# Kernel optimization log

Hardware: AMD Instinct MI355X
Metric: run time of the kernel (lower is better)

The kernel has to match this reference:

```python
import jax, jax.numpy as jnp
import numpy as np

N, E = 50000, 800000
NODE_DIM, EDGE_DIM, HIDDEN = 128, 32, 128


def setup_inputs() -> dict:
    key = jax.random.key(0)
    ks = jax.random.split(key, 12)
    def lin(k, fan_in, shape):
        bound = 1.0 / np.sqrt(fan_in)
        return jax.random.uniform(k, shape, jnp.float32, -bound, bound)
    return {
        "x": jax.random.normal(ks[0], (N, NODE_DIM), jnp.float32),
        "edge_index": jax.random.randint(ks[1], (2, E), 0, N),
        "edge_attr": jax.random.normal(ks[2], (E, EDGE_DIM), jnp.float32),
        # msg MLP: Linear(node+edge -> hidden), Linear(hidden -> hidden)
        "W1": lin(ks[3], NODE_DIM + EDGE_DIM, (HIDDEN, NODE_DIM + EDGE_DIM)),
        "b1": lin(ks[4], NODE_DIM + EDGE_DIM, (HIDDEN,)),
        "W2": lin(ks[5], HIDDEN, (HIDDEN, HIDDEN)),
        "b2": lin(ks[6], HIDDEN, (HIDDEN,)),
        # GRUCell(input=HIDDEN, hidden=NODE_DIM); gate order r,z,n (torch)
        "W_ih": lin(ks[7], NODE_DIM, (3 * NODE_DIM, HIDDEN)),
        "b_ih": lin(ks[8], NODE_DIM, (3 * NODE_DIM,)),
        "W_hh": lin(ks[9], NODE_DIM, (3 * NODE_DIM, NODE_DIM)),
        "b_hh": lin(ks[10], NODE_DIM, (3 * NODE_DIM,)),
    }


def reference(x, edge_index, edge_attr, W1, b1, W2, b2, W_ih, b_ih, W_hh, b_hh):
    src, dst = edge_index[0], edge_index[1]
    # gather + edge MLP: [E, node+edge] -> [E, hidden]
    m_in = jnp.concatenate([x[src], edge_attr], axis=-1)
    h1 = jax.nn.silu(m_in @ W1.T + b1)
    m = jax.nn.silu(h1 @ W2.T + b2)
    # scatter-add messages per destination node
    agg = jax.ops.segment_sum(m, dst, num_segments=x.shape[0])  # [N, hidden]
    # GRUCell: gates in torch order (r, z, n)
    gi = agg @ W_ih.T + b_ih  # [N, 3*node_dim]
    gh = x @ W_hh.T + b_hh
    i_r, i_z, i_n = jnp.split(gi, 3, axis=-1)
    h_r, h_z, h_n = jnp.split(gh, 3, axis=-1)
    r = jax.nn.sigmoid(i_r + h_r)
    z = jax.nn.sigmoid(i_z + h_z)
    n = jnp.tanh(i_n + r * h_n)
    return (1.0 - z) * n + z * x
```

## Files before the change

kernel.cpp:

```cpp
#include <hip/hip_runtime.h>
#include <hip/hip_bf16.h>
#include <cstdint>

typedef __bf16 bf16x8 __attribute__((ext_vector_type(8)));
typedef __bf16 bf16x4 __attribute__((ext_vector_type(4)));
typedef float  f32x4  __attribute__((ext_vector_type(4)));

#define ND 128
#define HID 128

__device__ __forceinline__ f32x4 mfma_bf16(bf16x8 a, bf16x8 b, f32x4 c) {
  return __builtin_amdgcn_mfma_f32_16x16x32_bf16(a, b, c, 0, 0, 0);
}
__device__ __forceinline__ float fast_sigmoid(float x) {
  return __fdividef(1.f, 1.f + __expf(-x));
}
__device__ __forceinline__ float fast_silu(float x) {
  return __fdividef(x, 1.f + __expf(-x));
}
__device__ __forceinline__ float fast_tanh(float x) {
  float cx = fminf(fmaxf(x, -15.f), 15.f);
  float e = __expf(2.f * cx);
  return __fdividef(e - 1.f, e + 1.f);
}

__global__ void cvt_f32_bf16(const float* __restrict__ src, __bf16* __restrict__ dst, int n8) {
  int i = blockIdx.x * blockDim.x + threadIdx.x;
  if (i >= n8) return;
  const float4* s = reinterpret_cast<const float4*>(src) + (size_t)i * 2;
  float4 a = s[0], b = s[1];
  bf16x8 v;
  v[0] = (__bf16)a.x; v[1] = (__bf16)a.y; v[2] = (__bf16)a.z; v[3] = (__bf16)a.w;
  v[4] = (__bf16)b.x; v[5] = (__bf16)b.y; v[6] = (__bf16)b.z; v[7] = (__bf16)b.w;
  reinterpret_cast<bf16x8*>(dst)[i] = v;
}

__global__ void k_hist(const int* __restrict__ dst, int* __restrict__ counts, int E) {
  int e = blockIdx.x * 256 + threadIdx.x;
  if (e < E) atomicAdd(&counts[dst[e]], 1);
}

__global__ void k_blocksum(const int* __restrict__ counts, int* __restrict__ bsum) {
  __shared__ int sd[256];
  int t = threadIdx.x;
  sd[t] = counts[blockIdx.x * 256 + t];
  __syncthreads();
  for (int d = 128; d > 0; d >>= 1) { if (t < d) sd[t] += sd[t + d]; __syncthreads(); }
  if (!t) bsum[blockIdx.x] = sd[0];
}

__global__ void k_scan_bsum(int* __restrict__ bsum, int nb) {
  __shared__ int sd[256];
  int t = threadIdx.x;
  int v = (t < nb) ? bsum[t] : 0;
  sd[t] = v;
  __syncthreads();
  for (int d = 1; d < 256; d <<= 1) {
    int u = (t >= d) ? sd[t - d] : 0;
    __syncthreads();
    sd[t] += u;
    __syncthreads();
  }
  if (t < nb) bsum[t] = sd[t] - v;
}

__global__ void k_scan_write(const int* __restrict__ counts, const int* __restrict__ bsum,
                             int* __restrict__ offsets, int* __restrict__ cursor) {
  __shared__ int sd[256];
  int t = threadIdx.x, b = blockIdx.x;
  int i = b * 256 + t;
  int c = counts[i];
  sd[t] = c;
  __syncthreads();
  for (int d = 1; d < 256; d <<= 1) {
    int u = (t >= d) ? sd[t - d] : 0;
    __syncthreads();
    sd[t] += u;
    __syncthreads();
  }
  int excl = bsum[b] + sd[t] - c;
  offsets[i] = excl;
  cursor[i]  = excl;
  if (b == (int)gridDim.x - 1 && t == 255) offsets[i + 1] = excl + c;
}

__global__ void k_spos(const int* __restrict__ dst, int* __restrict__ cursor,
                       int* __restrict__ spos, int E) {
  int e = blockIdx.x * 256 + threadIdx.x;
  if (e < E) spos[e] = atomicAdd(&cursor[dst[e]], 1);
}

#define TILE_E 64
#define A_PAD 168
#define H_PAD 136

template <int SORT>
__global__ __launch_bounds__(512) void edge_mlp(
    const __bf16* __restrict__ xb,
    const int*    __restrict__ ei,
    const float*  __restrict__ ea,
    const __bf16* __restrict__ W1b,
    const float*  __restrict__ b1,
    const __bf16* __restrict__ W2b,
    const float*  __restrict__ b2,
    float*  __restrict__ agg,
    __bf16* __restrict__ mbuf,
    const int* __restrict__ spos,
    int E, int ntiles)
{
  __shared__ __bf16 Als[TILE_E][A_PAD];
  __shared__ __bf16 H1ls[TILE_E][H_PAD];
  __shared__ int sposls[TILE_E];

  const int tid = threadIdx.x;
  const int w  = tid >> 6;
  const int l  = tid & 63;
  const int l4 = l >> 4;
  const int lm = l & 15;
  const int jw = w * 16 + lm;

  bf16x8 bw1[5];
#pragma unroll
  for (int kt = 0; kt < 5; ++kt)
    bw1[kt] = *reinterpret_cast<const bf16x8*>(W1b + (size_t)jw * 160 + kt * 32 + l4 * 8);
  bf16x8 bw2[4];
#pragma unroll
  for (int kt = 0; kt < 4; ++kt)
    bw2[kt] = *reinterpret_cast<const bf16x8*>(W2b + (size_t)jw * 128 + kt * 32 + l4 * 8);
  const float b1v = b1[jw];
  const float b2v = b2[jw];
  const int* srcp = ei;
  const int* dstp = ei + E;

  __bf16* Mls = &Als[0][0];

  for (int tile = blockIdx.x; tile < ntiles; tile += gridDim.x) {
    const int e0 = tile * TILE_E;

#pragma unroll
    for (int it = 0; it < 2; ++it) {
      int idx = it * 512 + tid;
      int e = idx >> 4, q = idx & 15;
      int s = srcp[e0 + e];
      bf16x8 v = *reinterpret_cast<const bf16x8*>(xb + (size_t)s * ND + q * 8);
      *reinterpret_cast<bf16x8*>(&Als[e][q * 8]) = v;
    }
    {
      int e = tid >> 3, q = tid & 7;
      float4 v = reinterpret_cast<const float4*>(ea)[(size_t)(e0 + e) * 8 + q];
      bf16x4 h;
      h[0] = (__bf16)v.x; h[1] = (__bf16)v.y; h[2] = (__bf16)v.z; h[3] = (__bf16)v.w;
      *reinterpret_cast<bf16x4*>(&Als[e][ND + q * 4]) = h;
    }
    if (SORT && tid < TILE_E) sposls[tid] = spos[e0 + tid];
    __syncthreads();

#pragma unroll
    for (int rt = 0; rt < 4; ++rt) {
      const int er = rt * 16;
      f32x4 acc = {0.f, 0.f, 0.f, 0.f};
#pragma unroll
      for (int kt = 0; kt < 5; ++kt) {
        bf16x8 a = *reinterpret_cast<const bf16x8*>(&Als[er + lm][kt * 32 + l4 * 8]);
        acc = mfma_bf16(a, bw1[kt], acc);
      }
#pragma unroll
      for (int rr = 0; rr < 4; ++rr) {
        float hv = fast_silu(acc[rr] + b1v);
        H1ls[er + l4 * 4 + rr][jw] = (__bf16)hv;
      }
    }
    __syncthreads();

#pragma unroll
    for (int rt = 0; rt < 4; ++rt) {
      const int er = rt * 16;
      f32x4 acc = {0.f, 0.f, 0.f, 0.f};
#pragma unroll
      for (int kt = 0; kt < 4; ++kt) {
        bf16x8 a = *reinterpret_cast<const bf16x8*>(&H1ls[er + lm][kt * 32 + l4 * 8]);
        acc = mfma_bf16(a, bw2[kt], acc);
      }
      if (SORT) {
#pragma unroll
        for (int rr = 0; rr < 4; ++rr) {
          float mv = fast_silu(acc[rr] + b2v);
          Mls[(er + l4 * 4 + rr) * H_PAD + jw] = (__bf16)mv;
        }
      } else {
#pragma unroll
        for (int rr = 0; rr < 4; ++rr) {
          float mv = fast_silu(acc[rr] + b2v);
          int d = dstp[e0 + er + l4 * 4 + rr];
          atomicAdd(agg + (size_t)d * HID + jw, mv);
        }
      }
    }
    __syncthreads();

    if (SORT) {
#pragma unroll
      for (int it = 0; it < 2; ++it) {
        int idx = it * 512 + tid;
        int row = idx >> 4, q = idx & 15;
        bf16x8 v = *reinterpret_cast<const bf16x8*>(&Mls[row * H_PAD + q * 8]);
        int sp = sposls[row];
        *reinterpret_cast<bf16x8*>(mbuf + (size_t)sp * HID + q * 8) = v;
      }
      __syncthreads();
    }
  }
}

__global__ __launch_bounds__(256) void k_aggregate(
    const __bf16* __restrict__ mbuf, const int* __restrict__ offsets,
    __bf16* __restrict__ aggb, int N)
{
  int node = blockIdx.x * 4 + (threadIdx.x >> 6);
  int l = threadIdx.x & 63;
  if (node >= N) return;
  int lo = offsets[node], hi = offsets[node + 1];
  float s0 = 0.f, s1 = 0.f;
  const uint32_t* p = reinterpret_cast<const uint32_t*>(mbuf) + (size_t)lo * 64 + l;
  int r = lo;
  for (; r + 1 < hi; r += 2) {
    uint32_t v0 = p[0];
    uint32_t v1 = p[64];
    p += 128;
    s0 += __uint_as_float(v0 << 16);
    s1 += __uint_as_float(v0 & 0xffff0000u);
    s0 += __uint_as_float(v1 << 16);
    s1 += __uint_as_float(v1 & 0xffff0000u);
  }
  if (r < hi) {
    uint32_t v0 = p[0];
    s0 += __uint_as_float(v0 << 16);
    s1 += __uint_as_float(v0 & 0xffff0000u);
  }
  uint32_t o = (uint32_t)__builtin_bit_cast(unsigned short, (__bf16)s0) |
               ((uint32_t)__builtin_bit_cast(unsigned short, (__bf16)s1) << 16);
  reinterpret_cast<uint32_t*>(aggb)[(size_t)node * 64 + l] = o;
}

__global__ __launch_bounds__(512) void gru2(
    const __bf16* __restrict__ aggb,
    const __bf16* __restrict__ xb,
    const float*  __restrict__ x,
    const __bf16* __restrict__ Wih, const float* __restrict__ bih,
    const __bf16* __restrict__ Whh, const float* __restrict__ bhh,
    float* __restrict__ out, int N)
{
  const int tid = threadIdx.x;
  const int w = tid >> 6, l = tid & 63;
  const int l4 = l >> 4, lm = l & 15;
  const int n0 = blockIdx.x * 64;
  const int jr = w * 16 + lm, jz = jr + 128, jn = jr + 256;

  bf16x8 WiR[4], WhR[4], WiZ[4], WhZ[4], WiN[4], WhN[4];
#pragma unroll
  for (int kt = 0; kt < 4; ++kt) {
    int ko = kt * 32 + l4 * 8;
    WiR[kt] = *reinterpret_cast<const bf16x8*>(Wih + (size_t)jr * ND + ko);
    WhR[kt] = *reinterpret_cast<const bf16x8*>(Whh + (size_t)jr * ND + ko);
    WiZ[kt] = *reinterpret_cast<const bf16x8*>(Wih + (size_t)jz * ND + ko);
    WhZ[kt] = *reinterpret_cast<const bf16x8*>(Whh + (size_t)jz * ND + ko);
    WiN[kt] = *reinterpret_cast<const bf16x8*>(Wih + (size_t)jn * ND + ko);
    WhN[kt] = *reinterpret_cast<const bf16x8*>(Whh + (size_t)jn * ND + ko);
  }
  const float bir = bih[jr] + bhh[jr];
  const float biz = bih[jz] + bhh[jz];
  const float bin = bih[jn], bhn = bhh[jn];

#pragma unroll
  for (int rt = 0; rt < 4; ++rt) {
    int na = n0 + rt * 16 + lm;
    bf16x8 aA[4], aX[4];
#pragma unroll
    for (int kt = 0; kt < 4; ++kt) {
      int ko = kt * 32 + l4 * 8;
      bf16x8 z8 = {};
      aA[kt] = (na < N) ? *reinterpret_cast<const bf16x8*>(aggb + (size_t)na * ND + ko) : z8;
      aX[kt] = (na < N) ? *reinterpret_cast<const bf16x8*>(xb + (size_t)na * ND + ko) : z8;
    }
    f32x4 aR = {0.f,0.f,0.f,0.f}, aZ = {0.f,0.f,0.f,0.f};
    f32x4 ai = {0.f,0.f,0.f,0.f}, ah = {0.f,0.f,0.f,0.f};
#pragma unroll
    for (int kt = 0; kt < 4; ++kt) {
      aR = mfma_bf16(aA[kt], WiR[kt], aR);
      aR = mfma_bf16(aX[kt], WhR[kt], aR);
      aZ = mfma_bf16(aA[kt], WiZ[kt], aZ);
      aZ = mfma_bf16(aX[kt], WhZ[kt], aZ);
      ai = mfma_bf16(aA[kt], WiN[kt], ai);
      ah = mfma_bf16(aX[kt], WhN[kt], ah);
    }
#pragma unroll
    for (int rr = 0; rr < 4; ++rr) {
      int node = n0 + rt * 16 + l4 * 4 + rr;
      if (node < N) {
        float r = fast_sigmoid(aR[rr] + bir);
        float z = fast_sigmoid(aZ[rr] + biz);
        float n = fast_tanh(ai[rr] + bin + r * (ah[rr] + bhn));
        float xv = x[(size_t)node * ND + jr];
        out[(size_t)node * ND + jr] = (1.f - z) * n + z * xv;
      }
    }
  }
}

extern "C" void kernel_launch(void* const* d_in, const int* in_sizes, int n_in,
                              void* d_out, int out_size, void* d_ws, size_t ws_size,
                              hipStream_t stream) {
  const float* x   = (const float*)d_in[0];
  const int*   ei  = (const int*)d_in[1];
  const float* ea  = (const float*)d_in[2];
  const float* W1  = (const float*)d_in[3];
  const float* b1  = (const float*)d_in[4];
  const float* W2  = (const float*)d_in[5];
  const float* b2  = (const float*)d_in[6];
  const float* Wih = (const float*)d_in[7];
  const float* bih = (const float*)d_in[8];
  const float* Whh = (const float*)d_in[9];
  const float* bhh = (const float*)d_in[10];
  float* out = (float*)d_out;
  const int N = in_sizes[0] / ND;
  const int E = in_sizes[1] / 2;

  const int nb = (N + 255) / 256;
  const int nC = nb * 256;

  char* ws = (char*)d_ws;
  size_t off = 0;
  auto alloc = [&](size_t bytes) -> void* {
    void* p = ws + off;
    off += (bytes + 255) & ~(size_t)255;
    return p;
  };
  __bf16* xb   = (__bf16*)alloc((size_t)N * ND * 2);
  __bf16* aggb = (__bf16*)alloc((size_t)N * ND * 2);
  __bf16* W1b  = (__bf16*)alloc(128 * 160 * 2);
  __bf16* W2b  = (__bf16*)alloc(128 * 128 * 2);
  __bf16* Wihb = (__bf16*)alloc(384 * 128 * 2);
  __bf16* Whhb = (__bf16*)alloc(384 * 128 * 2);
  size_t common_off = off;

  int*    counts  = (int*)alloc((size_t)nC * 4);
  int*    offsets = (int*)alloc((size_t)(nC + 16) * 4);
  int*    cursor  = (int*)alloc((size_t)nC * 4);
  int*    bsum    = (int*)alloc(256 * 4);
  int*    spos    = (int*)alloc((size_t)E * 4);
  __bf16* mbuf    = (__bf16*)alloc((size_t)E * HID * 2);
  size_t need_sort = off;

  bool use_sort = (ws_size >= need_sort);

  cvt_f32_bf16<<<(N * ND / 8 + 255) / 256, 256, 0, stream>>>(x, xb, N * ND / 8);
  cvt_f32_bf16<<<(128 * 160 / 8 + 255) / 256, 256, 0, stream>>>(W1, W1b, 128 * 160 / 8);
  cvt_f32_bf16<<<(128 * 128 / 8 + 255) / 256, 256, 0, stream>>>(W2, W2b, 128 * 128 / 8);
  cvt_f32_bf16<<<(384 * 128 / 8 + 255) / 256, 256, 0, stream>>>(Wih, Wihb, 384 * 128 / 8);
  cvt_f32_bf16<<<(384 * 128 / 8 + 255) / 256, 256, 0, stream>>>(Whh, Whhb, 384 * 128 / 8);

  const int ntiles = E / TILE_E;
  const int* dstp = ei + E;

  if (use_sort) {
    hipMemsetAsync(counts, 0, (size_t)nC * 4, stream);
    k_hist<<<(E + 255) / 256, 256, 0, stream>>>(dstp, counts, E);
    k_blocksum<<<nb, 256, 0, stream>>>(counts, bsum);
    k_scan_bsum<<<1, 256, 0, stream>>>(bsum, nb);
    k_scan_write<<<nb, 256, 0, stream>>>(counts, bsum, offsets, cursor);
    k_spos<<<(E + 255) / 256, 256, 0, stream>>>(dstp, cursor, spos, E);
    edge_mlp<1><<<2500, 512, 0, stream>>>(xb, ei, ea, W1b, b1, W2b, b2,
                                          nullptr, mbuf, spos, E, ntiles);
    k_aggregate<<<(N + 3) / 4, 256, 0, stream>>>(mbuf, offsets, aggb, N);
  } else {
    off = common_off;
    float* aggf = (float*)alloc((size_t)N * ND * 4);
    hipMemsetAsync(aggf, 0, (size_t)N * ND * 4, stream);
    edge_mlp<0><<<2500, 512, 0, stream>>>(xb, ei, ea, W1b, b1, W2b, b2,
                                          aggf, nullptr, nullptr, E, ntiles);
    cvt_f32_bf16<<<(N * ND / 8 + 255) / 256, 256, 0, stream>>>(aggf, aggb, N * ND / 8);
  }

  gru2<<<(N + 63) / 64, 512, 0, stream>>>(aggb, xb, x, Wihb, bih, Whhb, bhh, out, N);
}
```

Baseline: 387.8 us.

## Restructure edge MLP with swizzled LDS, transposed MFMA, fused conversions

The edge MLP now runs 256-thread blocks, each wave covering 32 output columns. It uses XOR-swizzled LDS layouts in place of padding and swaps the MFMA operands so each lane holds 4 consecutive output features. That lets the messages go straight to the sorted buffer as vector stores, which removes the extra LDS staging pass and one barrier. The five fp32-to-bf16 conversion launches are merged into one kernel. The aggregation loop is unrolled by 4, and the GRU kernel also uses transposed MFMA to get float4 bias loads and output stores. The wider per-wave tile roughly doubles the weight registers held, which may lower occupancy.

After: 378.8 us. -2.3%, faster.

```diff
diff --git a/kernel.cpp b/kernel.cpp
--- a/kernel.cpp
+++ b/kernel.cpp
@@ -24,15 +24,25 @@
   return __fdividef(e - 1.f, e + 1.f);
 }
 
-__global__ void cvt_f32_bf16(const float* __restrict__ src, __bf16* __restrict__ dst, int n8) {
+__global__ void cvt_all(const float* __restrict__ s0, __bf16* __restrict__ d0, int c1,
+                        const float* __restrict__ s1, __bf16* __restrict__ d1, int c2,
+                        const float* __restrict__ s2, __bf16* __restrict__ d2, int c3,
+                        const float* __restrict__ s3, __bf16* __restrict__ d3, int c4,
+                        const float* __restrict__ s4, __bf16* __restrict__ d4, int c5) {
   int i = blockIdx.x * blockDim.x + threadIdx.x;
-  if (i >= n8) return;
-  const float4* s = reinterpret_cast<const float4*>(src) + (size_t)i * 2;
-  float4 a = s[0], b = s[1];
+  const float* s; __bf16* d; int j;
+  if (i < c1)      { s = s0; d = d0; j = i; }
+  else if (i < c2) { s = s1; d = d1; j = i - c1; }
+  else if (i < c3) { s = s2; d = d2; j = i - c2; }
+  else if (i < c4) { s = s3; d = d3; j = i - c3; }
+  else if (i < c5) { s = s4; d = d4; j = i - c4; }
+  else return;
+  const float4* sp = reinterpret_cast<const float4*>(s) + (size_t)j * 2;
+  float4 a = sp[0], b = sp[1];
   bf16x8 v;
   v[0] = (__bf16)a.x; v[1] = (__bf16)a.y; v[2] = (__bf16)a.z; v[3] = (__bf16)a.w;
   v[4] = (__bf16)b.x; v[5] = (__bf16)b.y; v[6] = (__bf16)b.z; v[7] = (__bf16)b.w;
-  reinterpret_cast<bf16x8*>(dst)[i] = v;
+  reinterpret_cast<bf16x8*>(d)[j] = v;
 }
 
 __global__ void k_hist(const int* __restrict__ dst, int* __restrict__ counts, int E) {
@@ -91,11 +101,9 @@
 }
 
 #define TILE_E 64
-#define A_PAD 168
-#define H_PAD 136
 
 template <int SORT>
-__global__ __launch_bounds__(512) void edge_mlp(
+__global__ __launch_bounds__(256) void edge_mlp(
     const __bf16* __restrict__ xb,
     const int*    __restrict__ ei,
     const float*  __restrict__ ea,
@@ -108,107 +116,121 @@
     const int* __restrict__ spos,
     int E, int ntiles)
 {
-  __shared__ __bf16 Als[TILE_E][A_PAD];
-  __shared__ __bf16 H1ls[TILE_E][H_PAD];
+  __shared__ __bf16 Als[TILE_E * 192];
+  __shared__ __bf16 H1[TILE_E * 128];
   __shared__ int sposls[TILE_E];
+  char* AlsB = (char*)Als;
+  char* H1B  = (char*)H1;
 
   const int tid = threadIdx.x;
   const int w  = tid >> 6;
   const int l  = tid & 63;
   const int l4 = l >> 4;
   const int lm = l & 15;
-  const int jw = w * 16 + lm;
-
-  bf16x8 bw1[5];
-#pragma unroll
-  for (int kt = 0; kt < 5; ++kt)
-    bw1[kt] = *reinterpret_cast<const bf16x8*>(W1b + (size_t)jw * 160 + kt * 32 + l4 * 8);
-  bf16x8 bw2[4];
-#pragma unroll
-  for (int kt = 0; kt < 4; ++kt)
-    bw2[kt] = *reinterpret_cast<const bf16x8*>(W2b + (size_t)jw * 128 + kt * 32 + l4 * 8);
-  const float b1v = b1[jw];
-  const float b2v = b2[jw];
+  const int jb = w * 32;
+
+  bf16x8 bw1[2][5], bw2[2][4];
+#pragma unroll
+  for (int jt = 0; jt < 2; ++jt) {
+    const int jr = jb + jt * 16 + lm;
+#pragma unroll
+    for (int kt = 0; kt < 5; ++kt)
+      bw1[jt][kt] = *reinterpret_cast<const bf16x8*>(W1b + (size_t)jr * 160 + kt * 32 + l4 * 8);
+#pragma unroll
+    for (int kt = 0; kt < 4; ++kt)
+      bw2[jt][kt] = *reinterpret_cast<const bf16x8*>(W2b + (size_t)jr * 128 + kt * 32 + l4 * 8);
+  }
+  float4 b1v[2], b2v[2];
+#pragma unroll
+  for (int jt = 0; jt < 2; ++jt) {
+    b1v[jt] = *reinterpret_cast<const float4*>(b1 + jb + jt * 16 + l4 * 4);
+    b2v[jt] = *reinterpret_cast<const float4*>(b2 + jb + jt * 16 + l4 * 4);
+  }
   const int* srcp = ei;
   const int* dstp = ei + E;
 
-  __bf16* Mls = &Als[0][0];
-
   for (int tile = blockIdx.x; tile < ntiles; tile += gridDim.x) {
     const int e0 = tile * TILE_E;
 
 #pragma unroll
-    for (int it = 0; it < 2; ++it) {
-      int idx = it * 512 + tid;
+    for (int it = 0; it < 4; ++it) {
+      int idx = it * 256 + tid;
       int e = idx >> 4, q = idx & 15;
       int s = srcp[e0 + e];
       bf16x8 v = *reinterpret_cast<const bf16x8*>(xb + (size_t)s * ND + q * 8);
-      *reinterpret_cast<bf16x8*>(&Als[e][q * 8]) = v;
-    }
-    {
-      int e = tid >> 3, q = tid & 7;
+      *reinterpret_cast<bf16x8*>(AlsB + e * 384 + ((q ^ (e & 7)) << 4)) = v;
+    }
+#pragma unroll
+    for (int it = 0; it < 2; ++it) {
+      int idx = it * 256 + tid;
+      int e = idx >> 3, q = idx & 7;
       float4 v = reinterpret_cast<const float4*>(ea)[(size_t)(e0 + e) * 8 + q];
       bf16x4 h;
       h[0] = (__bf16)v.x; h[1] = (__bf16)v.y; h[2] = (__bf16)v.z; h[3] = (__bf16)v.w;
-      *reinterpret_cast<bf16x4*>(&Als[e][ND + q * 4]) = h;
+      int chunk = 16 + (q >> 1);
+      *reinterpret_cast<bf16x4*>(AlsB + e * 384 + ((chunk ^ (e & 7)) << 4) + ((q & 1) << 3)) = h;
     }
     if (SORT && tid < TILE_E) sposls[tid] = spos[e0 + tid];
     __syncthreads();
 
 #pragma unroll
-    for (int rt = 0; rt < 4; ++rt) {
-      const int er = rt * 16;
-      f32x4 acc = {0.f, 0.f, 0.f, 0.f};
+    for (int et = 0; et < 4; ++et) {
+      const int e = et * 16 + lm;
+      const int sw = (lm & 7);
+      f32x4 acc0 = {0.f, 0.f, 0.f, 0.f}, acc1 = {0.f, 0.f, 0.f, 0.f};
 #pragma unroll
       for (int kt = 0; kt < 5; ++kt) {
-        bf16x8 a = *reinterpret_cast<const bf16x8*>(&Als[er + lm][kt * 32 + l4 * 8]);
-        acc = mfma_bf16(a, bw1[kt], acc);
+        bf16x8 bfrag = *reinterpret_cast<const bf16x8*>(AlsB + e * 384 + (((kt * 4 + l4) ^ sw) << 4));
+        acc0 = mfma_bf16(bw1[0][kt], bfrag, acc0);
+        acc1 = mfma_bf16(bw1[1][kt], bfrag, acc1);
       }
+      bf16x4 h0, h1;
 #pragma unroll
       for (int rr = 0; rr < 4; ++rr) {
-        float hv = fast_silu(acc[rr] + b1v);
-        H1ls[er + l4 * 4 + rr][jw] = (__bf16)hv;
+        h0[rr] = (__bf16)fast_silu(acc0[rr] + (&b1v[0].x)[rr]);
+        h1[rr] = (__bf16)fast_silu(acc1[rr] + (&b1v[1].x)[rr]);
       }
-    }
-    __syncthreads();
-
-#pragma unroll
-    for (int rt = 0; rt < 4; ++rt) {
-      const int er = rt * 16;
-      f32x4 acc = {0.f, 0.f, 0.f, 0.f};
+      int c0 = (jb >> 3) + (l4 >> 1);
+      int inner = (l4 & 1) << 3;
+      *reinterpret_cast<bf16x4*>(H1B + e * 256 + ((c0 ^ sw) << 4) + inner) = h0;
+      *reinterpret_cast<bf16x4*>(H1B + e * 256 + (((c0 + 2) ^ sw) << 4) + inner) = h1;
+    }
+    __syncthreads();
+
+#pragma unroll
+    for (int et = 0; et < 4; ++et) {
+      const int e = et * 16 + lm;
+      const int sw = (lm & 7);
+      f32x4 acc0 = {0.f, 0.f, 0.f, 0.f}, acc1 = {0.f, 0.f, 0.f, 0.f};
 #pragma unroll
       for (int kt = 0; kt < 4; ++kt) {
-        bf16x8 a = *reinterpret_cast<const bf16x8*>(&H1ls[er + lm][kt * 32 + l4 * 8]);
-        acc = mfma_bf16(a, bw2[kt], acc);
+        bf16x8 bfrag = *reinterpret_cast<const bf16x8*>(H1B + e * 256 + (((kt * 4 + l4) ^ sw) << 4));
+        acc0 = mfma_bf16(bw2[0][kt], bfrag, acc0);
+        acc1 = mfma_bf16(bw2[1][kt], bfrag, acc1);
       }
       if (SORT) {
+        bf16x4 m0, m1;
 #pragma unroll
         for (int rr = 0; rr < 4; ++rr) {
-          float mv = fast_silu(acc[rr] + b2v);
-          Mls[(er + l4 * 4 + rr) * H_PAD + jw] = (__bf16)mv;
+          m0[rr] = (__bf16)fast_silu(acc0[rr] + (&b2v[0].x)[rr]);
+          m1[rr] = (__bf16)fast_silu(acc1[rr] + (&b2v[1].x)[rr]);
         }
+        int sp = sposls[e];
+        __bf16* rowp = mbuf + (size_t)sp * HID + jb + l4 * 4;
+        *reinterpret_cast<bf16x4*>(rowp)      = m0;
+        *reinterpret_cast<bf16x4*>(rowp + 16) = m1;
       } else {
+        int d = dstp[e0 + e];
 #pragma unroll
         for (int rr = 0; rr < 4; ++rr) {
-          float mv = fast_silu(acc[rr] + b2v);
-          int d = dstp[e0 + er + l4 * 4 + rr];
-          atomicAdd(agg + (size_t)d * HID + jw, mv);
+          atomicAdd(agg + (size_t)d * HID + jb + l4 * 4 + rr,
+                    fast_silu(acc0[rr] + (&b2v[0].x)[rr]));
+          atomicAdd(agg + (size_t)d * HID + jb + 16 + l4 * 4 + rr,
+                    fast_silu(acc1[rr] + (&b2v[1].x)[rr]));
         }
       }
     }
     __syncthreads();
-
-    if (SORT) {
-#pragma unroll
-      for (int it = 0; it < 2; ++it) {
-        int idx = it * 512 + tid;
-        int row = idx >> 4, q = idx & 15;
-        bf16x8 v = *reinterpret_cast<const bf16x8*>(&Mls[row * H_PAD + q * 8]);
-        int sp = sposls[row];
-        *reinterpret_cast<bf16x8*>(mbuf + (size_t)sp * HID + q * 8) = v;
-      }
-      __syncthreads();
-    }
   }
 }
 
@@ -220,22 +242,23 @@
   int l = threadIdx.x & 63;
   if (node >= N) return;
   int lo = offsets[node], hi = offsets[node + 1];
+  int cnt = hi - lo;
   float s0 = 0.f, s1 = 0.f;
   const uint32_t* p = reinterpret_cast<const uint32_t*>(mbuf) + (size_t)lo * 64 + l;
-  int r = lo;
-  for (; r + 1 < hi; r += 2) {
-    uint32_t v0 = p[0];
-    uint32_t v1 = p[64];
-    p += 128;
-    s0 += __uint_as_float(v0 << 16);
-    s1 += __uint_as_float(v0 & 0xffff0000u);
-    s0 += __uint_as_float(v1 << 16);
-    s1 += __uint_as_float(v1 & 0xffff0000u);
-  }
-  if (r < hi) {
-    uint32_t v0 = p[0];
-    s0 += __uint_as_float(v0 << 16);
-    s1 += __uint_as_float(v0 & 0xffff0000u);
+  int r = 0;
+  for (; r + 4 <= cnt; r += 4) {
+    uint32_t u0 = p[0], u1 = p[64], u2 = p[128], u3 = p[192];
+    p += 256;
+    s0 += __uint_as_float(u0 << 16) + __uint_as_float(u1 << 16)
+        + __uint_as_float(u2 << 16) + __uint_as_float(u3 << 16);
+    s1 += __uint_as_float(u0 & 0xffff0000u) + __uint_as_float(u1 & 0xffff0000u)
+        + __uint_as_float(u2 & 0xffff0000u) + __uint_as_float(u3 & 0xffff0000u);
+  }
+  for (; r < cnt; ++r) {
+    uint32_t u = p[0];
+    p += 64;
+    s0 += __uint_as_float(u << 16);
+    s1 += __uint_as_float(u & 0xffff0000u);
   }
   uint32_t o = (uint32_t)__builtin_bit_cast(unsigned short, (__bf16)s0) |
                ((uint32_t)__builtin_bit_cast(unsigned short, (__bf16)s1) << 16);
@@ -254,7 +277,8 @@
   const int w = tid >> 6, l = tid & 63;
   const int l4 = l >> 4, lm = l & 15;
   const int n0 = blockIdx.x * 64;
-  const int jr = w * 16 + lm, jz = jr + 128, jn = jr + 256;
+  const int jb = w * 16;
+  const int jr = jb + lm, jz = jr + 128, jn = jr + 256;
 
   bf16x8 WiR[4], WhR[4], WiZ[4], WhZ[4], WiN[4], WhN[4];
 #pragma unroll
@@ -267,42 +291,53 @@
     WiN[kt] = *reinterpret_cast<const bf16x8*>(Wih + (size_t)jn * ND + ko);
     WhN[kt] = *reinterpret_cast<const bf16x8*>(Whh + (size_t)jn * ND + ko);
   }
-  const float bir = bih[jr] + bhh[jr];
-  const float biz = bih[jz] + bhh[jz];
-  const float bin = bih[jn], bhn = bhh[jn];
+  float4 birv, bizv, binv, bhnv;
+  {
+    int j0 = jb + l4 * 4;
+    float4 a = *reinterpret_cast<const float4*>(bih + j0);
+    float4 b = *reinterpret_cast<const float4*>(bhh + j0);
+    birv = make_float4(a.x + b.x, a.y + b.y, a.z + b.z, a.w + b.w);
+    a = *reinterpret_cast<const float4*>(bih + 128 + j0);
+    b = *reinterpret_cast<const float4*>(bhh + 128 + j0);
+    bizv = make_float4(a.x + b.x, a.y + b.y, a.z + b.z, a.w + b.w);
+    binv = *reinterpret_cast<const float4*>(bih + 256 + j0);
+    bhnv = *reinterpret_cast<const float4*>(bhh + 256 + j0);
+  }
 
 #pragma unroll
   for (int rt = 0; rt < 4; ++rt) {
-    int na = n0 + rt * 16 + lm;
+    const int node = n0 + rt * 16 + lm;
+    const bool ok = node < N;
     bf16x8 aA[4], aX[4];
 #pragma unroll
     for (int kt = 0; kt < 4; ++kt) {
       int ko = kt * 32 + l4 * 8;
       bf16x8 z8 = {};
-      aA[kt] = (na < N) ? *reinterpret_cast<const bf16x8*>(aggb + (size_t)na * ND + ko) : z8;
-      aX[kt] = (na < N) ? *reinterpret_cast<const bf16x8*>(xb + (size_t)na * ND + ko) : z8;
+      aA[kt] = ok ? *reinterpret_cast<const bf16x8*>(aggb + (size_t)node * ND + ko) : z8;
+      aX[kt] = ok ? *reinterpret_cast<const bf16x8*>(xb + (size_t)node * ND + ko) : z8;
     }
     f32x4 aR = {0.f,0.f,0.f,0.f}, aZ = {0.f,0.f,0.f,0.f};
     f32x4 ai = {0.f,0.f,0.f,0.f}, ah = {0.f,0.f,0.f,0.f};
 #pragma unroll
     for (int kt = 0; kt < 4; ++kt) {
-      aR = mfma_bf16(aA[kt], WiR[kt], aR);
-      aR = mfma_bf16(aX[kt], WhR[kt], aR);
-      aZ = mfma_bf16(aA[kt], WiZ[kt], aZ);
-      aZ = mfma_bf16(aX[kt], WhZ[kt], aZ);
-      ai = mfma_bf16(aA[kt], WiN[kt], ai);
-      ah = mfma_bf16(aX[kt], WhN[kt], ah);
-    }
-#pragma unroll
-    for (int rr = 0; rr < 4; ++rr) {
-      int node = n0 + rt * 16 + l4 * 4 + rr;
-      if (node < N) {
-        float r = fast_sigmoid(aR[rr] + bir);
-        float z = fast_sigmoid(aZ[rr] + biz);
-        float n = fast_tanh(ai[rr] + bin + r * (ah[rr] + bhn));
-        float xv = x[(size_t)node * ND + jr];
-        out[(size_t)node * ND + jr] = (1.f - z) * n + z * xv;
+      aR = mfma_bf16(WiR[kt], aA[kt], aR);
+      aR = mfma_bf16(WhR[kt], aX[kt], aR);
+      aZ = mfma_bf16(WiZ[kt], aA[kt], aZ);
+      aZ = mfma_bf16(WhZ[kt], aX[kt], aZ);
+      ai = mfma_bf16(WiN[kt], aA[kt], ai);
+      ah = mfma_bf16(WhN[kt], aX[kt], ah);
+    }
+    if (ok) {
+      float4 xv = *reinterpret_cast<const float4*>(x + (size_t)node * ND + jb + l4 * 4);
+      float4 ov;
+#pragma unroll
+      for (int rr = 0; rr < 4; ++rr) {
+        float r = fast_sigmoid(aR[rr] + (&birv.x)[rr]);
+        float z = fast_sigmoid(aZ[rr] + (&bizv.x)[rr]);
+        float n = fast_tanh(ai[rr] + (&binv.x)[rr] + r * (ah[rr] + (&bhnv.x)[rr]));
+        (&ov.x)[rr] = (1.f - z) * n + z * (&xv.x)[rr];
       }
+      *reinterpret_cast<float4*>(out + (size_t)node * ND + jb + l4 * 4) = ov;
     }
   }
 }
@@ -353,11 +388,10 @@
 
   bool use_sort = (ws_size >= need_sort);
 
-  cvt_f32_bf16<<<(N * ND / 8 + 255) / 256, 256, 0, stream>>>(x, xb, N * ND / 8);
-  cvt_f32_bf16<<<(128 * 160 / 8 + 255) / 256, 256, 0, stream>>>(W1, W1b, 128 * 160 / 8);
-  cvt_f32_bf16<<<(128 * 128 / 8 + 255) / 256, 256, 0, stream>>>(W2, W2b, 128 * 128 / 8);
-  cvt_f32_bf16<<<(384 * 128 / 8 + 255) / 256, 256, 0, stream>>>(Wih, Wihb, 384 * 128 / 8);
-  cvt_f32_bf16<<<(384 * 128 / 8 + 255) / 256, 256, 0, stream>>>(Whh, Whhb, 384 * 128 / 8);
+  const int n8_x = N * ND / 8, n8_1 = 128 * 160 / 8, n8_2 = 128 * 128 / 8, n8_g = 384 * 128 / 8;
+  int c1 = n8_x, c2 = c1 + n8_1, c3 = c2 + n8_2, c4 = c3 + n8_g, c5 = c4 + n8_g;
+  cvt_all<<<(c5 + 255) / 256, 256, 0, stream>>>(x, xb, c1, W1, W1b, c2, W2, W2b, c3,
+                                                Wih, Wihb, c4, Whh, Whhb, c5);
 
   const int ntiles = E / TILE_E;
   const int* dstp = ei + E;
@@ -369,16 +403,20 @@
     k_scan_bsum<<<1, 256, 0, stream>>>(bsum, nb);
     k_scan_write<<<nb, 256, 0, stream>>>(counts, bsum, offsets, cursor);
     k_spos<<<(E + 255) / 256, 256, 0, stream>>>(dstp, cursor, spos, E);
-    edge_mlp<1><<<2500, 512, 0, stream>>>(xb, ei, ea, W1b, b1, W2b, b2,
+    edge_mlp<1><<<2500, 256, 0, stream>>>(xb, ei, ea, W1b, b1, W2b, b2,
                                           nullptr, mbuf, spos, E, ntiles);
     k_aggregate<<<(N + 3) / 4, 256, 0, stream>>>(mbuf, offsets, aggb, N);
   } else {
     off = common_off;
     float* aggf = (float*)alloc((size_t)N * ND * 4);
     hipMemsetAsync(aggf, 0, (size_t)N * ND * 4, stream);
-    edge_mlp<0><<<2500, 512, 0, stream>>>(xb, ei, ea, W1b, b1, W2b, b2,
+    edge_mlp<0><<<2500, 256, 0, stream>>>(xb, ei, ea, W1b, b1, W2b, b2,
                                           aggf, nullptr, nullptr, E, ntiles);
-    cvt_f32_bf16<<<(N * ND / 8 + 255) / 256, 256, 0, stream>>>(aggf, aggb, N * ND / 8);
+    cvt_all<<<(n8_x + 255) / 256, 256, 0, stream>>>(aggf, aggb, n8_x,
+                                                    nullptr, nullptr, n8_x,
+                                                    nullptr, nullptr, n8_x,
+                                                    nullptr, nullptr, n8_x,
+                                                    nullptr, nullptr, n8_x);
   }
 
   gru2<<<(N + 63) / 64, 512, 0, stream>>>(aggb, xb, x, Wihb, bih, Whhb, bhh, out, N);
```
